# Kernel tuning notes

Hardware: AMD Instinct MI355X
Metric: run time of the kernel (lower is better)

## Reference

```python
import jax, jax.numpy as jnp
import numpy as np

LN_EPS = 1e-5
SUM_EPS = 1e-6
Q_EPS = 1e-8

def layernorm(x):
    # parameter-free LayerNorm over last axis (elementwise_affine=False)
    mu = jnp.mean(x, axis=-1, keepdims=True)
    var = jnp.mean(jnp.square(x - mu), axis=-1, keepdims=True)
    return (x - mu) * jax.lax.rsqrt(var + LN_EPS)

def ternary_quant(W):
    # BitNet-b1.58-style ternary quantization: scale = mean(|W|), Wq in {-1,0,1}*scale
    scale = jnp.mean(jnp.abs(W))
    Wq = jnp.clip(jnp.round(W / (scale + Q_EPS)), -1.0, 1.0) * scale
    return Wq

def setup_inputs() -> dict:
    key = jax.random.key(0)
    ks = jax.random.split(key, 8)
    B, S, F = 8, 2048, 2048
    x = jax.random.normal(ks[0], (B, S, F), dtype=jnp.float32)
    seq_pos_code = jnp.arange(S, dtype=jnp.int32)
    feature_pos_code = jnp.arange(F, dtype=jnp.int32)
    # TernaryMLP(F, F, residual=False): ternary-quantized linear F -> F
    W_v = jax.random.normal(ks[1], (F, F), dtype=jnp.float32) * (1.0 / np.sqrt(F))
    b_v = jnp.zeros((F,), dtype=jnp.float32)
    # left attn: Linear(F, 1)
    w_left = jax.random.normal(ks[2], (F, 1), dtype=jnp.float32) * (1.0 / np.sqrt(F))
    b_left = jnp.zeros((1,), dtype=jnp.float32)
    # right attn: Linear(S, 1)
    w_right = jax.random.normal(ks[3], (S, 1), dtype=jnp.float32) * (1.0 / np.sqrt(S))
    b_right = jnp.zeros((1,), dtype=jnp.float32)
    alpha = jax.random.uniform(ks[4], (1,), dtype=jnp.float32)
    return {"x": x, "seq_pos_code": seq_pos_code, "feature_pos_code": feature_pos_code,
            "W_v": W_v, "b_v": b_v, "w_left": w_left, "b_left": b_left,
            "w_right": w_right, "b_right": b_right, "alpha": alpha}

def reference(x, seq_pos_code, feature_pos_code, W_v, b_v, w_left, b_left, w_right, b_right, alpha):
    B, S, F = x.shape
    # value path: ternary-quantized linear (TernaryMLP, residual=False)
    Wq = ternary_quant(W_v)
    v = jnp.einsum('bsf,fg->bsg', x, Wq) + b_v  # [B,S,F]
    # left attention: Linear(F->1) -> [B,S,1]; transpose; LN over S; ReLU; transpose back
    la = (jnp.einsum('bsf,fo->bso', x, w_left) + b_left)[..., 0]  # [B,S]
    la = jax.nn.relu(layernorm(la))[..., None]                    # [B,S,1]
    la = la / (jnp.sum(la, axis=-1, keepdims=True) + SUM_EPS)     # normalize over last dim (size 1)
    # right attention: transpose -> [B,F,S]; Linear(S->1); transpose -> [B,1,F]; LN over F; ReLU
    ra = (jnp.einsum('bsf,so->bfo', x, w_right) + b_right)[..., 0]  # [B,F]
    ra = jax.nn.relu(layernorm(ra))[:, None, :]                     # [B,1,F]
    ra = ra / (jnp.sum(ra, axis=-1, keepdims=True) + SUM_EPS)       # normalize over F
    a = alpha[0]
    return (1.0 - a) * x + a * la * v * ra
```

## Files before the change

kernel.cpp:

```cpp
#include <hip/hip_runtime.h>
#include <hip/hip_bf16.h>
#include <stdint.h>

#define B_ 8
#define S_ 2048
#define F_ 2048
#define M_ (B_*S_)
#define K_ F_
#define N_ F_

typedef __attribute__((ext_vector_type(4))) float f32x4;
typedef __attribute__((ext_vector_type(8))) short short8;

__device__ __forceinline__ unsigned short f2bf(float f){
  unsigned u = __float_as_uint(f);
  u += 0x7FFFu + ((u >> 16) & 1u);
  return (unsigned short)(u >> 16);
}

__device__ __forceinline__ void gload16(const void* g, const void* l){
  __builtin_amdgcn_global_load_lds(
      (const __attribute__((address_space(1))) void*)g,
      (__attribute__((address_space(3))) void*)l,
      16, 0, 0);
}

__device__ __forceinline__ float waveReduce(float v){
  #pragma unroll
  for (int off = 32; off; off >>= 1) v += __shfl_down(v, off, 64);
  return v;
}

__device__ __forceinline__ float blockReduceAll(float v, float* sbuf){
  v = waveReduce(v);
  int lane = threadIdx.x & 63, w = threadIdx.x >> 6;
  __syncthreads();
  if (lane == 0) sbuf[w] = v;
  __syncthreads();
  return sbuf[0] + sbuf[1] + sbuf[2] + sbuf[3];
}

__global__ __launch_bounds__(256) void k_abs1(const float* __restrict__ W, float* __restrict__ part){
  __shared__ float sb[4];
  size_t idx = ((size_t)blockIdx.x * 256 + threadIdx.x) * 4;
  f32x4 v = *(const f32x4*)(W + idx);
  float s = fabsf(v[0]) + fabsf(v[1]) + fabsf(v[2]) + fabsf(v[3]);
  s = blockReduceAll(s, sb);
  if (threadIdx.x == 0) part[blockIdx.x] = s;
}

__global__ __launch_bounds__(256) void k_abs2(const float* __restrict__ part, float* __restrict__ scalep){
  __shared__ float sb[4];
  float s = 0.f;
  int t = threadIdx.x;
  #pragma unroll
  for (int i = 0; i < 16; i++) s += part[t + i*256];
  s = blockReduceAll(s, sb);
  if (t == 0) scalep[0] = s * (1.0f / ((float)F_ * (float)F_));
}

__global__ __launch_bounds__(256) void k_quantT(const float* __restrict__ W, unsigned short* __restrict__ BT,
                                                const float* __restrict__ scalep){
  __shared__ float tile[32][33];
  int gx = blockIdx.x * 32;
  int fy = blockIdx.y * 32;
  int tx = threadIdx.x & 31, ty = threadIdx.x >> 5;
  float inv = 1.0f / (scalep[0] + 1e-8f);
  #pragma unroll
  for (int i = 0; i < 4; i++){
    int f = fy + ty + i*8;
    tile[ty + i*8][tx] = W[(size_t)f * F_ + gx + tx];
  }
  __syncthreads();
  #pragma unroll
  for (int i = 0; i < 4; i++){
    int g = gx + ty + i*8;
    float w = tile[tx][ty + i*8];
    float t = rintf(w * inv);
    t = fminf(1.0f, fmaxf(-1.0f, t));
    BT[(size_t)g * K_ + fy + tx] = f2bf(t);
  }
}

__global__ __launch_bounds__(256) void k_front(const float* __restrict__ X, const float* __restrict__ wl,
                                               const float* __restrict__ bl, const float* __restrict__ wrt,
                                               unsigned short* __restrict__ XH, float* __restrict__ la_raw,
                                               float* __restrict__ ra_raw){
  __shared__ float lap[4][32];
  int t = threadIdx.x, w = t >> 6, lane = t & 63;
  int r0 = blockIdx.x * 32;
  int b  = r0 >> 11;
  int f0 = t * 8;
  f32x4 wl0 = *(const f32x4*)(wl + f0);
  f32x4 wl1 = *(const f32x4*)(wl + f0 + 4);
  float racc[8];
  #pragma unroll
  for (int j = 0; j < 8; j++) racc[j] = 0.f;

  for (int rr = 0; rr < 32; rr += 2){
    int rowA = r0 + rr, rowB = r0 + rr + 1;
    const float* xrA = X + (size_t)rowA * F_ + f0;
    const float* xrB = X + (size_t)rowB * F_ + f0;
    f32x4 a0 = *(const f32x4*)(xrA);
    f32x4 a1 = *(const f32x4*)(xrA + 4);
    f32x4 b0 = *(const f32x4*)(xrB);
    f32x4 b1 = *(const f32x4*)(xrB + 4);
    ushort4 pa0, pa1, pb0, pb1;
    pa0.x = f2bf(a0[0]); pa0.y = f2bf(a0[1]); pa0.z = f2bf(a0[2]); pa0.w = f2bf(a0[3]);
    pa1.x = f2bf(a1[0]); pa1.y = f2bf(a1[1]); pa1.z = f2bf(a1[2]); pa1.w = f2bf(a1[3]);
    pb0.x = f2bf(b0[0]); pb0.y = f2bf(b0[1]); pb0.z = f2bf(b0[2]); pb0.w = f2bf(b0[3]);
    pb1.x = f2bf(b1[0]); pb1.y = f2bf(b1[1]); pb1.z = f2bf(b1[2]); pb1.w = f2bf(b1[3]);
    unsigned short* xhA = XH + (size_t)rowA * F_ + f0;
    unsigned short* xhB = XH + (size_t)rowB * F_ + f0;
    *(ushort4*)(xhA)     = pa0;
    *(ushort4*)(xhA + 4) = pa1;
    *(ushort4*)(xhB)     = pb0;
    *(ushort4*)(xhB + 4) = pb1;
    float dotA = a0[0]*wl0[0] + a0[1]*wl0[1] + a0[2]*wl0[2] + a0[3]*wl0[3]
               + a1[0]*wl1[0] + a1[1]*wl1[1] + a1[2]*wl1[2] + a1[3]*wl1[3];
    float dotB = b0[0]*wl0[0] + b0[1]*wl0[1] + b0[2]*wl0[2] + b0[3]*wl0[3]
               + b1[0]*wl1[0] + b1[1]*wl1[1] + b1[2]*wl1[2] + b1[3]*wl1[3];
    #pragma unroll
    for (int off = 32; off; off >>= 1){
      dotA += __shfl_down(dotA, off, 64);
      dotB += __shfl_down(dotB, off, 64);
    }
    if (lane == 0){ lap[w][rr] = dotA; lap[w][rr+1] = dotB; }
    float wsA = wrt[rowA & (S_-1)], wsB = wrt[rowB & (S_-1)];
    racc[0] += a0[0]*wsA + b0[0]*wsB; racc[1] += a0[1]*wsA + b0[1]*wsB;
    racc[2] += a0[2]*wsA + b0[2]*wsB; racc[3] += a0[3]*wsA + b0[3]*wsB;
    racc[4] += a1[0]*wsA + b1[0]*wsB; racc[5] += a1[1]*wsA + b1[1]*wsB;
    racc[6] += a1[2]*wsA + b1[2]*wsB; racc[7] += a1[3]*wsA + b1[3]*wsB;
  }
  __syncthreads();
  if (t < 32)
    la_raw[r0 + t] = lap[0][t] + lap[1][t] + lap[2][t] + lap[3][t] + bl[0];
  float* rb = ra_raw + b * F_ + f0;
  #pragma unroll
  for (int j = 0; j < 8; j++) atomicAdd(&rb[j], racc[j]);
}

__global__ __launch_bounds__(256) void k_ln(const float* __restrict__ la_raw, const float* __restrict__ ra_raw,
                                            const float* __restrict__ br, float* __restrict__ la,
                                            float* __restrict__ ra){
  __shared__ float sb[4];
  int blk = blockIdx.x;
  bool isRa = blk >= 8;
  int b = blk & 7;
  const float* p = isRa ? (ra_raw + b * F_) : (la_raw + b * S_);
  int t = threadIdx.x;
  float bb = isRa ? br[0] : 0.0f;
  float v[8]; float s = 0.f, s2 = 0.f;
  #pragma unroll
  for (int i = 0; i < 8; i++){ v[i] = p[t + i*256] + bb; s += v[i]; s2 += v[i]*v[i]; }
  s  = blockReduceAll(s,  sb);
  s2 = blockReduceAll(s2, sb);
  float mu  = s * (1.0f / 2048.0f);
  float var = s2 * (1.0f / 2048.0f) - mu*mu;
  float rstd = 1.0f / sqrtf(var + 1e-5f);
  float r[8]; float sr = 0.f;
  #pragma unroll
  for (int i = 0; i < 8; i++){ r[i] = fmaxf((v[i] - mu) * rstd, 0.0f); sr += r[i]; }
  if (isRa){
    sr = blockReduceAll(sr, sb);
    float invs = 1.0f / (sr + 1e-6f);
    #pragma unroll
    for (int i = 0; i < 8; i++) ra[b * F_ + t + i*256] = r[i] * invs;
  } else {
    #pragma unroll
    for (int i = 0; i < 8; i++) la[b * S_ + t + i*256] = r[i] / (r[i] + 1e-6f);
  }
}

__global__ __launch_bounds__(256) void k_gemm(
    const unsigned short* __restrict__ A, const unsigned short* __restrict__ BT,
    const float* __restrict__ X, const float* __restrict__ la, const float* __restrict__ ra,
    const float* __restrict__ bv, const float* __restrict__ alphap, const float* __restrict__ scalep,
    float* __restrict__ Out)
{
  __shared__ __align__(128) char lds[65536];
  const int NBX = N_ / 128;
  const int NT  = K_ / 32;
  int tid = threadIdx.x;
  int bid = blockIdx.x;
  const int nwg = (M_/128) * (N_/128);
  int cpx = nwg >> 3;
  int swz = (bid & 7) * cpx + (bid >> 3);
  int brow = swz / NBX, bcol = swz % NBX;
  int row0 = brow * 128, col0 = bcol * 128;

  int w = tid >> 6, lane = tid & 63;
  int wr = w >> 1, wc = w & 1;
  int lrow = lane & 15, kgrp = lane >> 4;

  f32x4 acc[4][4];
  #pragma unroll
  for (int m = 0; m < 4; m++)
    #pragma unroll
    for (int n = 0; n < 4; n++) acc[m][n] = (f32x4)(0.0f);

  int c0 = tid, c1 = tid + 256;
  int ar0 = c0 >> 2, ak0 = (((c0 & 3) ^ ((ar0 >> 1) & 3)) << 3);
  int ar1 = c1 >> 2, ak1 = (((c1 & 3) ^ ((ar1 >> 1) & 3)) << 3);
  const unsigned short* Ap0 = A  + (size_t)(row0 + ar0) * K_ + ak0;
  const unsigned short* Ap1 = A  + (size_t)(row0 + ar1) * K_ + ak1;
  const unsigned short* Bp0 = BT + (size_t)(col0 + ar0) * K_ + ak0;
  const unsigned short* Bp1 = BT + (size_t)(col0 + ar1) * K_ + ak1;
  int stoff = w * 1024;

  int aoff[4], boff[4];
  #pragma unroll
  for (int m = 0; m < 4; m++){
    int r  = wr*64 + m*16 + lrow;
    aoff[m] = r*64 + ((kgrp ^ ((r >> 1) & 3)) << 4);
    int rc = wc*64 + m*16 + lrow;
    boff[m] = 8192 + rc*64 + ((kgrp ^ ((rc >> 1) & 3)) << 4);
  }

#define STAGE(T) { \
    char* nb_ = lds + ((T) & 3) * 16384; \
    gload16(Ap0 + (size_t)(T)*32, nb_ + stoff); \
    gload16(Ap1 + (size_t)(T)*32, nb_ + 4096 + stoff); \
    gload16(Bp0 + (size_t)(T)*32, nb_ + 8192 + stoff); \
    gload16(Bp1 + (size_t)(T)*32, nb_ + 12288 + stoff); \
  }

  STAGE(0); STAGE(1); STAGE(2);
  asm volatile("s_waitcnt vmcnt(8)" ::: "memory");
  __builtin_amdgcn_s_barrier();

  for (int kt = 0; kt < NT; ++kt){
    if (kt + 3 < NT) STAGE(kt + 3);
    const char* bb = lds + (kt & 3) * 16384;
    short8 af[4], bfr[4];
    #pragma unroll
    for (int m = 0; m < 4; m++) af[m]  = *(const short8*)(bb + aoff[m]);
    #pragma unroll
    for (int n = 0; n < 4; n++) bfr[n] = *(const short8*)(bb + boff[n]);
    __builtin_amdgcn_s_setprio(1);
    #pragma unroll
    for (int m = 0; m < 4; m++)
      #pragma unroll
      for (int n = 0; n < 4; n++)
        acc[m][n] = __builtin_amdgcn_mfma_f32_16x16x32_bf16(af[m], bfr[n], acc[m][n], 0, 0, 0);
    __builtin_amdgcn_s_setprio(0);
    if (kt + 3 < NT)      { asm volatile("s_waitcnt vmcnt(8)" ::: "memory"); }
    else if (kt + 2 < NT) { asm volatile("s_waitcnt vmcnt(4)" ::: "memory"); }
    else if (kt + 1 < NT) { asm volatile("s_waitcnt vmcnt(0)" ::: "memory"); }
    if (kt + 1 < NT) __builtin_amdgcn_s_barrier();
  }
#undef STAGE

  float a = alphap[0];
  float scale = scalep[0];
  float oma = 1.0f - a;
  int bidx = row0 >> 11;
  const float* rab = ra + bidx * F_;
  #pragma unroll
  for (int m = 0; m < 4; m++){
    int rbase = row0 + wr*64 + m*16 + (lane >> 4) * 4;
    float lav[4];
    #pragma unroll
    for (int r = 0; r < 4; r++) lav[r] = la[rbase + r];
    #pragma unroll
    for (int n = 0; n < 4; n++){
      int col = col0 + wc*64 + n*16 + (lane & 15);
      float rav = rab[col];
      float bvv = bv[col];
      #pragma unroll
      for (int r = 0; r < 4; r++){
        int row = rbase + r;
        float v = acc[m][n][r] * scale + bvv;
        size_t idx = (size_t)row * N_ + col;
        Out[idx] = oma * X[idx] + a * lav[r] * v * rav;
      }
    }
  }
}

extern "C" void kernel_launch(void* const* d_in, const int* in_sizes, int n_in,
                              void* d_out, int out_size, void* d_ws, size_t ws_size,
                              hipStream_t stream){
  const float* x     = (const float*)d_in[0];
  const float* Wv    = (const float*)d_in[3];
  const float* bv    = (const float*)d_in[4];
  const float* wl    = (const float*)d_in[5];
  const float* bl    = (const float*)d_in[6];
  const float* wrt   = (const float*)d_in[7];
  const float* br    = (const float*)d_in[8];
  const float* alpha = (const float*)d_in[9];
  float* out = (float*)d_out;

  char* ws = (char*)d_ws;
  unsigned short* XH = (unsigned short*)(ws);
  unsigned short* BT = (unsigned short*)(ws + 67108864);
  float* la_raw = (float*)(ws + 75497472);
  float* la     = (float*)(ws + 75563008);
  float* ra_raw = (float*)(ws + 75628544);
  float* ra     = (float*)(ws + 75694080);
  float* part   = (float*)(ws + 75759616);
  float* scalep = (float*)(ws + 75776000);

  hipMemsetAsync(ra_raw, 0, B_ * F_ * sizeof(float), stream);
  k_abs1<<<4096, 256, 0, stream>>>(Wv, part);
  k_abs2<<<1, 256, 0, stream>>>(part, scalep);
  k_quantT<<<dim3(F_/32, F_/32), 256, 0, stream>>>(Wv, BT, scalep);
  k_front<<<M_/32, 256, 0, stream>>>(x, wl, bl, wrt, XH, la_raw, ra_raw);
  k_ln<<<16, 256, 0, stream>>>(la_raw, ra_raw, br, la, ra);
  k_gemm<<<2048, 256, 0, stream>>>(XH, BT, x, la, ra, bv, alpha, scalep, out);
}
```

Before: 465.8 us.

## Enlarge GEMM tile to 256x256 with 512 threads; fold scale reduction into atomics

The bf16 MFMA GEMM moves from 128x128 tiles with 4 waves to 256x256 tiles with 8 waves. Each wave now covers 128x64 of the output, and the four-stage LDS ring doubles to 128KB. This cuts global and LDS traffic per FLOP and halves the number of workgroups, but uses more registers per thread and allows fewer resident blocks per CU. Separately, the two-pass |W| mean reduction becomes a single kernel that does per-block atomicAdd into a zeroed scalar, with the normalisation moved to the consumers. k_front now collects all 32 row dot products first and then runs their wave shuffles together.

```diff
diff --git a/kernel.cpp b/kernel.cpp
--- a/kernel.cpp
+++ b/kernel.cpp
@@ -40,23 +40,13 @@
   return sbuf[0] + sbuf[1] + sbuf[2] + sbuf[3];
 }
 
-__global__ __launch_bounds__(256) void k_abs1(const float* __restrict__ W, float* __restrict__ part){
+__global__ __launch_bounds__(256) void k_abs1(const float* __restrict__ W, float* __restrict__ scalep){
   __shared__ float sb[4];
   size_t idx = ((size_t)blockIdx.x * 256 + threadIdx.x) * 4;
   f32x4 v = *(const f32x4*)(W + idx);
   float s = fabsf(v[0]) + fabsf(v[1]) + fabsf(v[2]) + fabsf(v[3]);
   s = blockReduceAll(s, sb);
-  if (threadIdx.x == 0) part[blockIdx.x] = s;
-}
-
-__global__ __launch_bounds__(256) void k_abs2(const float* __restrict__ part, float* __restrict__ scalep){
-  __shared__ float sb[4];
-  float s = 0.f;
-  int t = threadIdx.x;
-  #pragma unroll
-  for (int i = 0; i < 16; i++) s += part[t + i*256];
-  s = blockReduceAll(s, sb);
-  if (t == 0) scalep[0] = s * (1.0f / ((float)F_ * (float)F_));
+  if (threadIdx.x == 0) atomicAdd(scalep, s);
 }
 
 __global__ __launch_bounds__(256) void k_quantT(const float* __restrict__ W, unsigned short* __restrict__ BT,
@@ -65,7 +55,8 @@
   int gx = blockIdx.x * 32;
   int fy = blockIdx.y * 32;
   int tx = threadIdx.x & 31, ty = threadIdx.x >> 5;
-  float inv = 1.0f / (scalep[0] + 1e-8f);
+  float scale = scalep[0] * (1.0f / ((float)F_ * (float)F_));
+  float inv = 1.0f / (scale + 1e-8f);
   #pragma unroll
   for (int i = 0; i < 4; i++){
     int f = fy + ty + i*8;
@@ -93,44 +84,37 @@
   int f0 = t * 8;
   f32x4 wl0 = *(const f32x4*)(wl + f0);
   f32x4 wl1 = *(const f32x4*)(wl + f0 + 4);
+  float dots[32];
   float racc[8];
   #pragma unroll
   for (int j = 0; j < 8; j++) racc[j] = 0.f;
 
-  for (int rr = 0; rr < 32; rr += 2){
-    int rowA = r0 + rr, rowB = r0 + rr + 1;
-    const float* xrA = X + (size_t)rowA * F_ + f0;
-    const float* xrB = X + (size_t)rowB * F_ + f0;
-    f32x4 a0 = *(const f32x4*)(xrA);
-    f32x4 a1 = *(const f32x4*)(xrA + 4);
-    f32x4 b0 = *(const f32x4*)(xrB);
-    f32x4 b1 = *(const f32x4*)(xrB + 4);
-    ushort4 pa0, pa1, pb0, pb1;
-    pa0.x = f2bf(a0[0]); pa0.y = f2bf(a0[1]); pa0.z = f2bf(a0[2]); pa0.w = f2bf(a0[3]);
-    pa1.x = f2bf(a1[0]); pa1.y = f2bf(a1[1]); pa1.z = f2bf(a1[2]); pa1.w = f2bf(a1[3]);
-    pb0.x = f2bf(b0[0]); pb0.y = f2bf(b0[1]); pb0.z = f2bf(b0[2]); pb0.w = f2bf(b0[3]);
-    pb1.x = f2bf(b1[0]); pb1.y = f2bf(b1[1]); pb1.z = f2bf(b1[2]); pb1.w = f2bf(b1[3]);
-    unsigned short* xhA = XH + (size_t)rowA * F_ + f0;
-    unsigned short* xhB = XH + (size_t)rowB * F_ + f0;
-    *(ushort4*)(xhA)     = pa0;
-    *(ushort4*)(xhA + 4) = pa1;
-    *(ushort4*)(xhB)     = pb0;
-    *(ushort4*)(xhB + 4) = pb1;
-    float dotA = a0[0]*wl0[0] + a0[1]*wl0[1] + a0[2]*wl0[2] + a0[3]*wl0[3]
-               + a1[0]*wl1[0] + a1[1]*wl1[1] + a1[2]*wl1[2] + a1[3]*wl1[3];
-    float dotB = b0[0]*wl0[0] + b0[1]*wl0[1] + b0[2]*wl0[2] + b0[3]*wl0[3]
-               + b1[0]*wl1[0] + b1[1]*wl1[1] + b1[2]*wl1[2] + b1[3]*wl1[3];
-    #pragma unroll
-    for (int off = 32; off; off >>= 1){
-      dotA += __shfl_down(dotA, off, 64);
-      dotB += __shfl_down(dotB, off, 64);
-    }
-    if (lane == 0){ lap[w][rr] = dotA; lap[w][rr+1] = dotB; }
-    float wsA = wrt[rowA & (S_-1)], wsB = wrt[rowB & (S_-1)];
-    racc[0] += a0[0]*wsA + b0[0]*wsB; racc[1] += a0[1]*wsA + b0[1]*wsB;
-    racc[2] += a0[2]*wsA + b0[2]*wsB; racc[3] += a0[3]*wsA + b0[3]*wsB;
-    racc[4] += a1[0]*wsA + b1[0]*wsB; racc[5] += a1[1]*wsA + b1[1]*wsB;
-    racc[6] += a1[2]*wsA + b1[2]*wsB; racc[7] += a1[3]*wsA + b1[3]*wsB;
+  #pragma unroll
+  for (int rr = 0; rr < 32; ++rr){
+    int row = r0 + rr;
+    const float* xr = X + (size_t)row * F_ + f0;
+    f32x4 v0 = *(const f32x4*)(xr);
+    f32x4 v1 = *(const f32x4*)(xr + 4);
+    ushort4 p0, p1;
+    p0.x = f2bf(v0[0]); p0.y = f2bf(v0[1]); p0.z = f2bf(v0[2]); p0.w = f2bf(v0[3]);
+    p1.x = f2bf(v1[0]); p1.y = f2bf(v1[1]); p1.z = f2bf(v1[2]); p1.w = f2bf(v1[3]);
+    unsigned short* xh = XH + (size_t)row * F_ + f0;
+    *(ushort4*)(xh)     = p0;
+    *(ushort4*)(xh + 4) = p1;
+    dots[rr] = v0[0]*wl0[0] + v0[1]*wl0[1] + v0[2]*wl0[2] + v0[3]*wl0[3]
+             + v1[0]*wl1[0] + v1[1]*wl1[1] + v1[2]*wl1[2] + v1[3]*wl1[3];
+    float wsr = wrt[row & (S_-1)];
+    racc[0] += v0[0]*wsr; racc[1] += v0[1]*wsr; racc[2] += v0[2]*wsr; racc[3] += v0[3]*wsr;
+    racc[4] += v1[0]*wsr; racc[5] += v1[1]*wsr; racc[6] += v1[2]*wsr; racc[7] += v1[3]*wsr;
+  }
+  #pragma unroll
+  for (int off = 32; off; off >>= 1){
+    #pragma unroll
+    for (int rr = 0; rr < 32; ++rr) dots[rr] += __shfl_down(dots[rr], off, 64);
+  }
+  if (lane == 0){
+    #pragma unroll
+    for (int rr = 0; rr < 32; ++rr) lap[w][rr] = dots[rr];
   }
   __syncthreads();
   if (t < 32)
@@ -172,57 +156,59 @@
   }
 }
 
-__global__ __launch_bounds__(256) void k_gemm(
+__global__ __launch_bounds__(512, 2) void k_gemm(
     const unsigned short* __restrict__ A, const unsigned short* __restrict__ BT,
     const float* __restrict__ X, const float* __restrict__ la, const float* __restrict__ ra,
     const float* __restrict__ bv, const float* __restrict__ alphap, const float* __restrict__ scalep,
     float* __restrict__ Out)
 {
-  __shared__ __align__(128) char lds[65536];
-  const int NBX = N_ / 128;
+  __shared__ __align__(128) char lds[131072];
+  const int NBX = N_ / 256;
   const int NT  = K_ / 32;
   int tid = threadIdx.x;
   int bid = blockIdx.x;
-  const int nwg = (M_/128) * (N_/128);
+  const int nwg = (M_/256) * (N_/256);
   int cpx = nwg >> 3;
   int swz = (bid & 7) * cpx + (bid >> 3);
   int brow = swz / NBX, bcol = swz % NBX;
-  int row0 = brow * 128, col0 = bcol * 128;
+  int row0 = brow * 256, col0 = bcol * 256;
 
   int w = tid >> 6, lane = tid & 63;
-  int wr = w >> 1, wc = w & 1;
+  int wr = w >> 2, wc = w & 3;
   int lrow = lane & 15, kgrp = lane >> 4;
 
-  f32x4 acc[4][4];
-  #pragma unroll
-  for (int m = 0; m < 4; m++)
+  f32x4 acc[8][4];
+  #pragma unroll
+  for (int m = 0; m < 8; m++)
     #pragma unroll
     for (int n = 0; n < 4; n++) acc[m][n] = (f32x4)(0.0f);
 
-  int c0 = tid, c1 = tid + 256;
-  int ar0 = c0 >> 2, ak0 = (((c0 & 3) ^ ((ar0 >> 1) & 3)) << 3);
-  int ar1 = c1 >> 2, ak1 = (((c1 & 3) ^ ((ar1 >> 1) & 3)) << 3);
-  const unsigned short* Ap0 = A  + (size_t)(row0 + ar0) * K_ + ak0;
-  const unsigned short* Ap1 = A  + (size_t)(row0 + ar1) * K_ + ak1;
-  const unsigned short* Bp0 = BT + (size_t)(col0 + ar0) * K_ + ak0;
-  const unsigned short* Bp1 = BT + (size_t)(col0 + ar1) * K_ + ak1;
+  int ar0 = tid >> 2;
+  int q0  = ((tid & 3) ^ ((ar0 >> 1) & 3)) << 3;
+  const unsigned short* Ap0 = A  + (size_t)(row0 + ar0      ) * K_ + q0;
+  const unsigned short* Ap1 = A  + (size_t)(row0 + ar0 + 128) * K_ + q0;
+  const unsigned short* Bp0 = BT + (size_t)(col0 + ar0      ) * K_ + q0;
+  const unsigned short* Bp1 = BT + (size_t)(col0 + ar0 + 128) * K_ + q0;
   int stoff = w * 1024;
 
-  int aoff[4], boff[4];
-  #pragma unroll
-  for (int m = 0; m < 4; m++){
-    int r  = wr*64 + m*16 + lrow;
+  int aoff[8], boff[4];
+  #pragma unroll
+  for (int m = 0; m < 8; m++){
+    int r  = wr*128 + m*16 + lrow;
     aoff[m] = r*64 + ((kgrp ^ ((r >> 1) & 3)) << 4);
-    int rc = wc*64 + m*16 + lrow;
-    boff[m] = 8192 + rc*64 + ((kgrp ^ ((rc >> 1) & 3)) << 4);
+  }
+  #pragma unroll
+  for (int n = 0; n < 4; n++){
+    int rc = wc*64 + n*16 + lrow;
+    boff[n] = 16384 + rc*64 + ((kgrp ^ ((rc >> 1) & 3)) << 4);
   }
 
 #define STAGE(T) { \
-    char* nb_ = lds + ((T) & 3) * 16384; \
+    char* nb_ = lds + ((T) & 3) * 32768; \
     gload16(Ap0 + (size_t)(T)*32, nb_ + stoff); \
-    gload16(Ap1 + (size_t)(T)*32, nb_ + 4096 + stoff); \
-    gload16(Bp0 + (size_t)(T)*32, nb_ + 8192 + stoff); \
-    gload16(Bp1 + (size_t)(T)*32, nb_ + 12288 + stoff); \
+    gload16(Ap1 + (size_t)(T)*32, nb_ + 8192 + stoff); \
+    gload16(Bp0 + (size_t)(T)*32, nb_ + 16384 + stoff); \
+    gload16(Bp1 + (size_t)(T)*32, nb_ + 24576 + stoff); \
   }
 
   STAGE(0); STAGE(1); STAGE(2);
@@ -231,15 +217,15 @@
 
   for (int kt = 0; kt < NT; ++kt){
     if (kt + 3 < NT) STAGE(kt + 3);
-    const char* bb = lds + (kt & 3) * 16384;
-    short8 af[4], bfr[4];
-    #pragma unroll
-    for (int m = 0; m < 4; m++) af[m]  = *(const short8*)(bb + aoff[m]);
+    const char* bb = lds + (kt & 3) * 32768;
+    short8 af[8], bfr[4];
+    #pragma unroll
+    for (int m = 0; m < 8; m++) af[m]  = *(const short8*)(bb + aoff[m]);
     #pragma unroll
     for (int n = 0; n < 4; n++) bfr[n] = *(const short8*)(bb + boff[n]);
     __builtin_amdgcn_s_setprio(1);
     #pragma unroll
-    for (int m = 0; m < 4; m++)
+    for (int m = 0; m < 8; m++)
       #pragma unroll
       for (int n = 0; n < 4; n++)
         acc[m][n] = __builtin_amdgcn_mfma_f32_16x16x32_bf16(af[m], bfr[n], acc[m][n], 0, 0, 0);
@@ -252,19 +238,19 @@
 #undef STAGE
 
   float a = alphap[0];
-  float scale = scalep[0];
+  float scale = scalep[0] * (1.0f / ((float)F_ * (float)F_));
   float oma = 1.0f - a;
   int bidx = row0 >> 11;
   const float* rab = ra + bidx * F_;
   #pragma unroll
-  for (int m = 0; m < 4; m++){
-    int rbase = row0 + wr*64 + m*16 + (lane >> 4) * 4;
+  for (int m = 0; m < 8; m++){
+    int rbase = row0 + wr*128 + m*16 + kgrp * 4;
     float lav[4];
     #pragma unroll
     for (int r = 0; r < 4; r++) lav[r] = la[rbase + r];
     #pragma unroll
     for (int n = 0; n < 4; n++){
-      int col = col0 + wc*64 + n*16 + (lane & 15);
+      int col = col0 + wc*64 + n*16 + lrow;
       float rav = rab[col];
       float bvv = bv[col];
       #pragma unroll
@@ -294,18 +280,16 @@
   char* ws = (char*)d_ws;
   unsigned short* XH = (unsigned short*)(ws);
   unsigned short* BT = (unsigned short*)(ws + 67108864);
-  float* la_raw = (float*)(ws + 75497472);
-  float* la     = (float*)(ws + 75563008);
-  float* ra_raw = (float*)(ws + 75628544);
-  float* ra     = (float*)(ws + 75694080);
-  float* part   = (float*)(ws + 75759616);
-  float* scalep = (float*)(ws + 75776000);
-
-  hipMemsetAsync(ra_raw, 0, B_ * F_ * sizeof(float), stream);
-  k_abs1<<<4096, 256, 0, stream>>>(Wv, part);
-  k_abs2<<<1, 256, 0, stream>>>(part, scalep);
+  float* ra_raw = (float*)(ws + 75497472);
+  float* scalep = (float*)(ws + 75563008);
+  float* la_raw = (float*)(ws + 75563264);
+  float* la     = (float*)(ws + 75628800);
+  float* ra     = (float*)(ws + 75694336);
+
+  hipMemsetAsync(ra_raw, 0, 65536 + 256, stream);
+  k_abs1<<<4096, 256, 0, stream>>>(Wv, scalep);
   k_quantT<<<dim3(F_/32, F_/32), 256, 0, stream>>>(Wv, BT, scalep);
   k_front<<<M_/32, 256, 0, stream>>>(x, wl, bl, wrt, XH, la_raw, ra_raw);
   k_ln<<<16, 256, 0, stream>>>(la_raw, ra_raw, br, la, ra);
-  k_gemm<<<2048, 256, 0, stream>>>(XH, BT, x, la, ra, bv, alpha, scalep, out);
-}
+  k_gemm<<<512, 512, 0, stream>>>(XH, BT, x, la, ra, bv, alpha, scalep, out);
+}
```

Result: slower. 487.5 us (+4.7%).
